# Kernel optimization log

Measured on AMD Instinct MI355X. Metric: run time of the kernel, lower is better.

The kernel has to match this reference:

```python
import jax, jax.numpy as jnp
import numpy as np

H_IMG, W_IMG = 60, 80          # hardcoded grid in get_positional_encodings
NUM_HEADS = 8
DIM = 256
N_TOK = H_IMG * W_IMG          # 4800

# Hardcoded intrinsics in the source: fx=517/9, fy=517/8, cx=40, cy=30.
# fx_norm = fx/(2*cx)*2, fy_norm = fy/(2*cy)*2 ; cx_norm = cy_norm = 0,
# so Kinv is diagonal and Kinv @ [x, y, 1] = [x/fx_n, y/fy_n, 1].
_FX_N = (517.0 / 9.0) / 80.0 * 2.0
_FY_N = (517.0 / 8.0) / 60.0 * 2.0


def _positional(B):
    ys = jnp.linspace(-1.0, 1.0, H_IMG)
    xs = jnp.linspace(-1.0, 1.0, W_IMG)
    # loop index j*w + k: y varies over rows (outer), x over cols (inner)
    p3 = jnp.repeat(ys, W_IMG) / _FY_N   # (N,) = y'/w'
    p4 = jnp.tile(xs, H_IMG) / _FX_N     # (N,) = x'/w'
    pos = jnp.stack([p3 * p3, p4 * p4, p3 * p4, p3, p4, jnp.ones_like(p3)], axis=-1)  # (N,6)
    return jnp.broadcast_to(pos, (B, N_TOK, 6))


def setup_inputs() -> dict:
    key = jax.random.key(0)
    k1, k2, k3, k4, k5 = jax.random.split(key, 5)
    B, N, C, H = 1, N_TOK, DIM, NUM_HEADS
    return {
        "x1": jax.random.normal(k1, (B, N, C), dtype=jnp.float32),
        "x2": jax.random.normal(k2, (B, N, C), dtype=jnp.float32),
        "qkv_w": jax.random.normal(k3, (3 * C, C), dtype=jnp.float32) * 0.02,
        "proj_w": jax.random.normal(k4, (C, C + 6 * H), dtype=jnp.float32) * 0.02,
        "proj_b": jax.random.normal(k5, (C,), dtype=jnp.float32) * 0.02,
    }


def reference(x1, x2, qkv_w, proj_w, proj_b):
    B, N, C = x1.shape
    H = NUM_HEADS
    hd = C // H
    scale = hd ** -0.5
    D = hd + 6

    def qkv(x):
        y = (x @ qkv_w.T).reshape(B, N, 3, H, hd).transpose(2, 0, 3, 1, 4)
        return y[0], y[1], y[2]   # each (B,H,N,hd)

    q1, k1, v1 = qkv(x1)
    q2, k2, v2 = qkv(x2)

    pos_h = jnp.broadcast_to(_positional(B)[:, None], (B, H, N, 6))

    def fundamental(q, k, v):
        a = jnp.einsum('bhnd,bhmd->bhnm', q, k) * scale          # (B,H,N,N)
        af = jax.nn.softmax(a, axis=-1) * jax.nn.softmax(a, axis=-2)  # dual softmax
        vc = jnp.concatenate([v, pos_h], axis=-1)                 # (B,H,N,D)
        f = jnp.einsum('bhnc,bhnm->bhcm', vc, af)                 # V^T A
        f = jnp.einsum('bhcm,bhmd->bhcd', f, vc)                  # (V^T A) V -> (B,H,D,D)
        f = f.reshape(B, H * D, D).transpose(0, 2, 1)             # (B, D, H*D)
        return f @ proj_w.T + proj_b                              # (B, D, C)

    fundamental_1 = fundamental(q2, k1, v1)
    fundamental_2 = fundamental(q1, k2, v2)
    return fundamental_2, fundamental_1
```

## Files before the change

### kernel.cpp

```cpp
#include <hip/hip_runtime.h>
#include <stdint.h>
#include <math.h>

#define N_TOK 4800
#define NH 8
#define HD 32
#define DP 40
#define DD 38
#define NTILES 150
#define MCHUNK 3
#define FRAG 2048
#define SCALE 0.17677669529663687f
#define QSCALE (0.17677669529663687f * 1.4426950408889634f)

typedef float f32x16 __attribute__((ext_vector_type(16)));
typedef short s8v __attribute__((ext_vector_type(8)));
typedef int i2v __attribute__((ext_vector_type(2)));

#if __has_builtin(__builtin_amdgcn_exp2f)
#define EXP2F(x) __builtin_amdgcn_exp2f(x)
#else
#define EXP2F(x) exp2f(x)
#endif

__device__ __forceinline__ unsigned short f2bf(float x) {
    union { float f; uint32_t u; } v; v.f = x;
    uint32_t r = v.u + 0x7FFFu + ((v.u >> 16) & 1u);
    return (unsigned short)(r >> 16);
}
__device__ __forceinline__ int cvtpk(float lo, float hi) {
    int r;
    asm("v_cvt_pk_bf16_f32 %0, %1, %2" : "=v"(r) : "v"(lo), "v"(hi));
    return r;
}
__device__ __forceinline__ s8v mk_s8(int a, int b, int c, int d) {
    union { int i[4]; s8v s; } u;
    u.i[0] = a; u.i[1] = b; u.i[2] = c; u.i[3] = d;
    return u.s;
}
__device__ __forceinline__ float posv(int m, int idx) {
    const int rrow = m / 80, rcol = m % 80;
    const float y = -1.0f + (float)rrow * (2.0f / 59.0f);
    const float x = -1.0f + (float)rcol * (2.0f / 79.0f);
    const float p3 = y * (240.0f / 517.0f);
    const float p4 = x * (360.0f / 517.0f);
    if (idx == 0) return p3 * p3;
    if (idx == 1) return p4 * p4;
    if (idx == 2) return p3 * p4;
    if (idx == 3) return p3;
    if (idx == 4) return p4;
    return 1.0f;
}

template<int NX, int NY, int NZ>
__device__ __forceinline__ void swzdec(int& x, int& y, int& z) {
    const int L = blockIdx.x + NX * (blockIdx.y + NY * blockIdx.z);
    constexpr int cpx = NX * NY * NZ / 8;
    const int s = (L & 7) * cpx + (L >> 3);
    x = s % NX;
    const int r = s / NX;
    y = r % NY;
    z = r / NY;
}
template<int NX, int NY, int NZ>
__device__ __forceinline__ void swzdec_xo(int& x, int& y, int& z) {
    const int L = blockIdx.x + NX * (blockIdx.y + NY * blockIdx.z);
    constexpr int cpx = NX * NY * NZ / 8;
    const int s = (L & 7) * cpx + (L >> 3);
    x = s / (NY * NZ);
    const int r = s % (NY * NZ);
    y = r % NY;
    z = r / NY;
}

#define MFMA(a, b, c) __builtin_amdgcn_mfma_f32_32x32x16_bf16((a), (b), (c), 0, 0, 0)

__global__ __launch_bounds__(256) void frag_kernel(
    const float* __restrict__ x1, unsigned short* __restrict__ xh1,
    const float* __restrict__ x2, unsigned short* __restrict__ xh2,
    const float* __restrict__ w, unsigned short* __restrict__ wh)
{
    int b = blockIdx.x;
    const float* src; unsigned short* dh;
    if (b < 150)      { src = x1 + b * 8192; dh = xh1 + b * 8192; }
    else if (b < 300) { b -= 150; src = x2 + b * 8192; dh = xh2 + b * 8192; }
    else              { b -= 300; src = w + b * 8192; dh = wh + b * 8192; }
    const int t = threadIdx.x;
#pragma unroll
    for (int k = 0; k < 4; ++k) {
        const int f = k * 256 + t;
        const int c = f >> 6;
        const int rem = f & 63;
        const float* sp = src + (rem & 31) * 256 + c * 16 + (rem >> 5) * 8;
        const float4 a = *(const float4*)(sp);
        const float4 bb = *(const float4*)(sp + 4);
        const float vv[8] = {a.x, a.y, a.z, a.w, bb.x, bb.y, bb.z, bb.w};
        union { unsigned short s[8]; s8v v; } H;
#pragma unroll
        for (int j = 0; j < 8; ++j) H.s[j] = f2bf(vv[j]);
        *(s8v*)(dh + f * 8) = H.v;
    }
}

__global__ __launch_bounds__(128, 4) void qkv_mfma_kernel(
    const unsigned short* __restrict__ xhA, unsigned short* __restrict__ qbA,
    unsigned short* __restrict__ kbA, float* __restrict__ vcbA,
    const unsigned short* __restrict__ xhB, unsigned short* __restrict__ qbB,
    unsigned short* __restrict__ kbB, float* __restrict__ vcbB,
    const unsigned short* __restrict__ wh)
{
    __shared__ float tlbuf[2][32][33];
    int bx, by, bz;
    swzdec_xo<75, 12, 2>(bx, by, bz);
    const int sel = bz;
    const unsigned short* xh = sel ? xhB : xhA;
    unsigned short* qb = sel ? qbB : qbA;
    unsigned short* kb = sel ? kbB : kbA;
    float* vcb = sel ? vcbB : vcbA;
    const int lane = threadIdx.x & 63;
    const int wid = threadIdx.x >> 6;
    const int xtile = bx * 2 + wid;
    const unsigned short* xp = xh + (size_t)xtile * 8192 + lane * 8;
    const unsigned short* wp0 = wh + (size_t)(by * 2) * 8192 + lane * 8;
    const unsigned short* wp1 = wp0 + 8192;
    f32x16 acc0 = {}, acc1 = {};
#pragma unroll
    for (int c = 0; c < 16; ++c) {
        const s8v aH = *(const s8v*)(xp + c * 512);
        const s8v b0 = *(const s8v*)(wp0 + c * 512);
        const s8v b1 = *(const s8v*)(wp1 + c * 512);
        acc0 = MFMA(aH, b0, acc0);
        acc1 = MFMA(aH, b1, acc1);
    }
    const int lr = lane & 31, hi5 = lane >> 5;
    const int row = lane >> 1, ch = (lane & 1) * 16;
    float (*T)[33] = tlbuf[wid];
#pragma unroll
    for (int jj = 0; jj < 2; ++jj) {
#pragma unroll
        for (int r = 0; r < 16; ++r) {
            const float v = jj ? acc1[r] : acc0[r];
            T[(r & 3) + 8 * (r >> 2) + 4 * hi5][lr] = v;
        }
        const int jt = by * 2 + jj, s = jt >> 3, h = jt & 7;
        const int n = xtile * 32 + row;
        if (s == 2) {
            float4* dst = (float4*)&vcb[(size_t)(h * N_TOK + n) * HD + ch];
#pragma unroll
            for (int k = 0; k < 4; ++k) {
                dst[k] = make_float4(T[row][ch + 4 * k + 0], T[row][ch + 4 * k + 1],
                                     T[row][ch + 4 * k + 2], T[row][ch + 4 * k + 3]);
            }
        } else {
            const float m = (s == 0) ? QSCALE : 1.0f;
            unsigned short* dst = (s == 0 ? qb : kb)
                                  + (size_t)(h * N_TOK + n) * HD + ch;
            union { unsigned short u[8]; s8v v; } o0, o1;
#pragma unroll
            for (int i = 0; i < 8; ++i) {
                o0.u[i] = f2bf(T[row][ch + i] * m);
                o1.u[i] = f2bf(T[row][ch + 8 + i] * m);
            }
            *(s8v*)dst = o0.v;
            *(s8v*)(dst + 8) = o1.v;
        }
    }
}

__global__ __launch_bounds__(192, 4) void cs_kernel(
    const unsigned short* __restrict__ qbA, const unsigned short* __restrict__ kbA,
    float* __restrict__ csA,
    const unsigned short* __restrict__ qbB, const unsigned short* __restrict__ kbB,
    float* __restrict__ csB)
{
    int bx, by, bz;
    swzdec<50, 5, 16>(bx, by, bz);
    const int sel = bz >> 3;
    const unsigned short* qb = sel ? qbB : qbA;
    const unsigned short* kb = sel ? kbB : kbA;
    float* cs = sel ? csB : csA;
    const int lane = threadIdx.x & 63;
    const int wid = threadIdx.x >> 6;
    const int h = bz & 7;
    const int m0 = bx * 96 + wid * 32;
    const int lr = lane & 31, hi5 = lane >> 5;
    const int hbase = h * N_TOK;
    const unsigned short* kp = kb + (hbase + m0 + lr) * HD + 8 * hi5;
    const s8v bK0 = *(const s8v*)(kp);
    const s8v bK1 = *(const s8v*)(kp + 16);
    const unsigned short* qp = qb + (hbase + by * 960 + lr) * HD + 8 * hi5;
    s8v a0 = *(const s8v*)(qp);
    s8v a1 = *(const s8v*)(qp + 16);
    float csa = 0.f, csb = 0.f;
#pragma unroll 2
    for (int it = 0; it < 30; ++it) {
        qp += 32 * HD;
        const s8v na0 = *(const s8v*)(qp);
        const s8v na1 = *(const s8v*)(qp + 16);
        f32x16 acc = {};
        acc = MFMA(a0, bK0, acc);
        acc = MFMA(a1, bK1, acc);
#pragma unroll
        for (int r = 0; r < 16; r += 2) {
            csa += EXP2F(acc[r]);
            csb += EXP2F(acc[r + 1]);
        }
        a0 = na0; a1 = na1;
    }
    float csacc = csa + csb;
    csacc += __shfl_xor(csacc, 32);
    if (lane < 32) atomicAdd(&cs[hbase + m0 + lane], csacc);
}

__global__ __launch_bounds__(256) void vfrag_kernel(
    const float* __restrict__ vcA, const float* __restrict__ csA,
    unsigned short* __restrict__ vfA,
    const float* __restrict__ vcB, const float* __restrict__ csB,
    unsigned short* __restrict__ vfB)
{
    const int sel = blockIdx.y >> 3;
    const float* vc = sel ? vcB : vcA;
    const float* cs = sel ? csB : csA;
    unsigned short* vf = sel ? vfB : vfA;
    __shared__ float vl[32][33];
    __shared__ float ul[32];
    const int mt = blockIdx.x;
    const int h = blockIdx.y & 7;
    const int t = threadIdx.x;
    const int m0 = mt * 32;
    const float* vcbase = vc + (size_t)(h * N_TOK + m0) * HD;
    for (int e = t; e < 32 * HD; e += 256) vl[e >> 5][e & 31] = vcbase[e];
    if (t < 32) ul[t] = 1.0f / cs[(size_t)h * N_TOK + m0 + t];
    __syncthreads();
    const int b = t >> 6, lane = t & 63;
    const int hi5 = lane >> 5, lr = lane & 31;
    const int d = (b >> 1) * 32 + lr;
    const int mb = (b & 1) * 16 + hi5 * 8;
    union { unsigned short s[8]; s8v v; } pk;
#pragma unroll
    for (int j = 0; j < 8; ++j) {
        const int mo = mb + j;
        float v;
        if (d < 32)      v = vl[mo][d];
        else if (d < 38) v = posv(m0 + mo, d - 32);
        else             v = 0.0f;
        pk.s[j] = f2bf(v * ul[mo]);
    }
    *(s8v*)(vf + ((size_t)(h * NTILES + mt) * 4 + b) * 512 + lane * 8) = pk.v;
}

__global__ __launch_bounds__(192, 4) void tprime_mfma_kernel(
    const unsigned short* __restrict__ qbA, const unsigned short* __restrict__ kbA,
    const unsigned short* __restrict__ vfA, float* __restrict__ rsA,
    float* __restrict__ TA0, float* __restrict__ TA1, float* __restrict__ TA2,
    const unsigned short* __restrict__ qbB, const unsigned short* __restrict__ kbB,
    const unsigned short* __restrict__ vfB, float* __restrict__ rsB,
    float* __restrict__ TB0, float* __restrict__ TB1, float* __restrict__ TB2)
{
    int bx, by, bz;
    swzdec<50, MCHUNK, 16>(bx, by, bz);
    const int sel = bz >> 3;
    const unsigned short* qb = sel ? qbB : qbA;
    const unsigned short* kb = sel ? kbB : kbA;
    const unsigned short* vf = sel ? vfB : vfA;
    float* rs = sel ? rsB : rsA;
    float* T = sel ? (by == 0 ? TB0 : (by == 1 ? TB1 : TB2))
                   : (by == 0 ? TA0 : (by == 1 ? TA1 : TA2));
    const int lane = threadIdx.x & 63;
    const int wid = threadIdx.x >> 6;
    const int h = bz & 7;
    const int n0 = bx * 96 + wid * 32;
    const int lr = lane & 31, hi5 = lane >> 5;
    const int hbase = h * N_TOK;
    const unsigned short* qp = qb + (hbase + n0 + lr) * HD + 8 * hi5;
    const s8v bQ0 = *(const s8v*)(qp);
    const s8v bQ1 = *(const s8v*)(qp + 16);
    f32x16 t0 = {}, t1 = {};
    float rsa = 0.f, rsb = 0.f;
    const int mt0 = by * 50;
    const unsigned short* kp = kb + (hbase + mt0 * 32 + lr) * HD + 8 * hi5;
    const unsigned short* vp = vf + (size_t)(h * NTILES + mt0) * FRAG + lane * 8;
    s8v a0 = *(const s8v*)(kp);
    s8v a1 = *(const s8v*)(kp + 16);
    s8v v00 = *(const s8v*)(vp);
    s8v v01 = *(const s8v*)(vp + 512);
    s8v v10 = *(const s8v*)(vp + 1024);
    s8v v11 = *(const s8v*)(vp + 1536);
#pragma unroll 2
    for (int it = 0; it < 50; ++it) {
        kp += 32 * HD; vp += FRAG;
        const s8v na0 = *(const s8v*)(kp);
        const s8v na1 = *(const s8v*)(kp + 16);
        const s8v nv00 = *(const s8v*)(vp);
        const s8v nv01 = *(const s8v*)(vp + 512);
        const s8v nv10 = *(const s8v*)(vp + 1024);
        const s8v nv11 = *(const s8v*)(vp + 1536);
        f32x16 s = {};
        s = MFMA(a0, bQ0, s);
        s = MFMA(a1, bQ1, s);
        float p[16];
#pragma unroll
        for (int r = 0; r < 16; r += 2) {
            const float e0 = EXP2F(s[r]);
            const float e1 = EXP2F(s[r + 1]);
            rsa += e0; rsb += e1;
            p[r] = e0 * e0; p[r + 1] = e1 * e1;
        }
        const int L0 = cvtpk(p[0], p[1]),   L1 = cvtpk(p[2], p[3]);
        const int H0 = cvtpk(p[4], p[5]),   H1 = cvtpk(p[6], p[7]);
        const int L2 = cvtpk(p[8], p[9]),   L3 = cvtpk(p[10], p[11]);
        const int H2 = cvtpk(p[12], p[13]), H3 = cvtpk(p[14], p[15]);
        const i2v s0 = __builtin_amdgcn_permlane32_swap(L0, H0, false, false);
        const i2v s1 = __builtin_amdgcn_permlane32_swap(L1, H1, false, false);
        const i2v s2 = __builtin_amdgcn_permlane32_swap(L2, H2, false, false);
        const i2v s3 = __builtin_amdgcn_permlane32_swap(L3, H3, false, false);
        const s8v pa0 = mk_s8(s0[0], s1[0], s0[1], s1[1]);
        const s8v pa1 = mk_s8(s2[0], s3[0], s2[1], s3[1]);
        __builtin_amdgcn_s_setprio(1);
        t0 = MFMA(pa0, v00, t0);
        t0 = MFMA(pa1, v01, t0);
        t1 = MFMA(pa0, v10, t1);
        t1 = MFMA(pa1, v11, t1);
        __builtin_amdgcn_s_setprio(0);
        a0 = na0; a1 = na1;
        v00 = nv00; v01 = nv01; v10 = nv10; v11 = nv11;
    }
    float rsacc = rsa + rsb;
    rsacc += __shfl_xor(rsacc, 32);
    if (lane < 32) atomicAdd(&rs[hbase + n0 + lane], rsacc);
#pragma unroll
    for (int r = 0; r < 16; ++r) {
        const int n = n0 + (r & 3) + 8 * (r >> 2) + 4 * hi5;
        T[(size_t)(hbase + n) * DP + lr] = t0[r];
    }
    if (lr < 8) {
#pragma unroll
        for (int r = 0; r < 16; ++r) {
            const int n = n0 + (r & 3) + 8 * (r >> 2) + 4 * hi5;
            T[(size_t)(hbase + n) * DP + 32 + lr] = t1[r];
        }
    }
}

__global__ __launch_bounds__(256) void fgemm_kernel(
    const float* __restrict__ VCA, const float* __restrict__ rsA,
    const float* __restrict__ TA0, const float* __restrict__ TA1,
    const float* __restrict__ TA2, float* __restrict__ fA,
    const float* __restrict__ VCB, const float* __restrict__ rsB,
    const float* __restrict__ TB0, const float* __restrict__ TB1,
    const float* __restrict__ TB2, float* __restrict__ fB)
{
    const int sel = blockIdx.x >> 3;
    const float* VC = sel ? VCB : VCA;
    const float* rs = sel ? rsB : rsA;
    const float* Ta = sel ? TB0 : TA0;
    const float* Tb = sel ? TB1 : TA1;
    const float* Tc = sel ? TB2 : TA2;
    float* f = sel ? fB : fA;
    __shared__ __align__(16) float wvcl[64 * DP];
    __shared__ __align__(16) float tl[64 * DP];
    __shared__ float wl[64];
    const int h = blockIdx.x & 7, n0 = blockIdx.y * 64;
    const int t = threadIdx.x;
    if (t < 64) wl[t] = 1.0f / rs[(size_t)h * N_TOK + n0 + t];
    __syncthreads();
    const float* vcbase = VC + (size_t)(h * N_TOK + n0) * HD;
    const float* tabase = Ta + (size_t)(h * N_TOK + n0) * DP;
    const float* tbbase = Tb + (size_t)(h * N_TOK + n0) * DP;
    const float* tcbase = Tc + (size_t)(h * N_TOK + n0) * DP;
    for (int e = t; e < 64 * DP; e += 256) {
        const int row = e / DP, c = e - row * DP;
        float v;
        if (c < 32)      v = vcbase[row * HD + c];
        else if (c < 38) v = posv(n0 + row, c - 32);
        else             v = 0.0f;
        wvcl[e] = v * wl[row];
        tl[e] = tabase[e] + tbbase[e] + tcbase[e];
    }
    __syncthreads();
    for (int p = t; p < DD * DD; p += 256) {
        const int c = p / DD, d = p % DD;
        float s = 0.f;
#pragma unroll 8
        for (int n = 0; n < 64; ++n) s += wvcl[n * DP + c] * tl[n * DP + d];
        atomicAdd(&f[(size_t)(h * DD + c) * DP + d], s);
    }
}

__global__ __launch_bounds__(256) void out_kernel(
    const float* __restrict__ f1, const float* __restrict__ f2,
    const float* __restrict__ pw, const float* __restrict__ pb,
    float* __restrict__ out)
{
    const int sel = blockIdx.y;
    const float* f = sel ? f2 : f1;
    float* dst = sel ? out : (out + DD * 256);
    __shared__ __align__(16) float flds[304];
    const int d = blockIdx.x, t = threadIdx.x;
    for (int j = t; j < 304; j += 256) flds[j] = f[(size_t)j * DP + d];
    __syncthreads();
    float acc = pb[t];
    const float* pwrow = pw + (size_t)t * 304;
#pragma unroll 4
    for (int j = 0; j < 304; j += 4) {
        const float4 p4 = *(const float4*)&pwrow[j];
        const float4 f4 = *(const float4*)&flds[j];
        acc += p4.x * f4.x + p4.y * f4.y + p4.z * f4.z + p4.w * f4.w;
    }
    dst[(size_t)d * 256 + t] = acc;
}

extern "C" void kernel_launch(void* const* d_in, const int* in_sizes, int n_in,
                              void* d_out, int out_size, void* d_ws, size_t ws_size,
                              hipStream_t stream)
{
    const float* x1 = (const float*)d_in[0];
    const float* x2 = (const float*)d_in[1];
    const float* qkv_w = (const float*)d_in[2];
    const float* proj_w = (const float*)d_in[3];
    const float* proj_b = (const float*)d_in[4];
    float* out = (float*)d_out;

    const size_t QSZ = (size_t)NH * N_TOK * HD;
    const size_t VSZ = (size_t)NH * N_TOK * DP;
    const size_t SSZ = (size_t)NH * N_TOK;
    const size_t FSZ = (size_t)NH * DD * DP;
    const size_t XSZ = (size_t)N_TOK * 256;
    const size_t WSZ = (size_t)768 * 256;
    const size_t VTSZ = (size_t)NH * NTILES * FRAG;

    float* vc1 = (float*)d_ws;
    float* vc2 = vc1 + QSZ;
    float* rs1 = vc2 + QSZ;
    float* cs1 = rs1 + SSZ;
    float* rs2 = cs1 + SSZ;
    float* cs2 = rs2 + SSZ;
    float* f1 = cs2 + SSZ;
    float* f2 = f1 + FSZ;
    float* T1a = f2 + FSZ;
    float* T1b = T1a + VSZ;
    float* T1c = T1b + VSZ;
    float* T2a = T1c + VSZ;
    float* T2b = T2a + VSZ;
    float* T2c = T2b + VSZ;
    unsigned short* xh1 = (unsigned short*)(T2c + VSZ);
    unsigned short* xh2 = xh1 + XSZ;
    unsigned short* wh = xh2 + XSZ;
    unsigned short* qb1 = wh + WSZ;
    unsigned short* kb1 = qb1 + QSZ;
    unsigned short* qb2 = kb1 + QSZ;
    unsigned short* kb2 = qb2 + QSZ;
    unsigned short* vf1 = kb2 + QSZ;
    unsigned short* vf2 = vf1 + VTSZ;

    const size_t zbytes = (4 * SSZ + 2 * FSZ) * sizeof(float);
    hipMemsetAsync(rs1, 0, zbytes, stream);

    frag_kernel<<<324, 256, 0, stream>>>(x1, xh1, x2, xh2, qkv_w, wh);

    qkv_mfma_kernel<<<dim3(75, 12, 2), 128, 0, stream>>>(
        xh1, qb1, kb1, vc1, xh2, qb2, kb2, vc2, wh);

    cs_kernel<<<dim3(50, 5, 16), 192, 0, stream>>>(qb2, kb1, cs1,
                                                   qb1, kb2, cs2);
    vfrag_kernel<<<dim3(150, 16), 256, 0, stream>>>(vc1, cs1, vf1,
                                                    vc2, cs2, vf2);
    tprime_mfma_kernel<<<dim3(50, MCHUNK, 16), 192, 0, stream>>>(
        qb2, kb1, vf1, rs1, T1a, T1b, T1c,
        qb1, kb2, vf2, rs2, T2a, T2b, T2c);
    fgemm_kernel<<<dim3(16, 75), 256, 0, stream>>>(
        vc1, rs1, T1a, T1b, T1c, f1,
        vc2, rs2, T2a, T2b, T2c, f2);
    out_kernel<<<dim3(38, 2), 256, 0, stream>>>(f1, f2, proj_w, proj_b, out);
}
```

Measured before the change: 221.4 us.

## Store T partials in bf16, fold memset into frag kernel, widen cs tiles

The T partial buffers written by tprime and read by fgemm are now stored as packed bf16 instead of fp32, which halves that intermediate traffic at some cost in accumulation precision. The hipMemsetAsync is replaced by extra blocks in frag_kernel that zero the accumulator buffers, removing one launch. cs_kernel now handles 64 key columns per wave with two MFMA accumulators, halving the grid and reusing each Q fragment load twice.

```diff
diff --git a/kernel.cpp b/kernel.cpp
--- a/kernel.cpp
+++ b/kernel.cpp
@@ -27,6 +27,10 @@
     union { float f; uint32_t u; } v; v.f = x;
     uint32_t r = v.u + 0x7FFFu + ((v.u >> 16) & 1u);
     return (unsigned short)(r >> 16);
+}
+__device__ __forceinline__ float bf2f(unsigned short h) {
+    union { uint32_t u; float f; } v; v.u = ((uint32_t)h) << 16;
+    return v.f;
 }
 __device__ __forceinline__ int cvtpk(float lo, float hi) {
     int r;
@@ -78,14 +82,20 @@
 __global__ __launch_bounds__(256) void frag_kernel(
     const float* __restrict__ x1, unsigned short* __restrict__ xh1,
     const float* __restrict__ x2, unsigned short* __restrict__ xh2,
-    const float* __restrict__ w, unsigned short* __restrict__ wh)
+    const float* __restrict__ w, unsigned short* __restrict__ wh,
+    float* __restrict__ zbase, int zn4)
 {
     int b = blockIdx.x;
+    const int t = threadIdx.x;
+    if (b >= 324) {
+        const int i = (b - 324) * 256 + t;
+        if (i < zn4) ((float4*)zbase)[i] = make_float4(0.f, 0.f, 0.f, 0.f);
+        return;
+    }
     const float* src; unsigned short* dh;
     if (b < 150)      { src = x1 + b * 8192; dh = xh1 + b * 8192; }
     else if (b < 300) { b -= 150; src = x2 + b * 8192; dh = xh2 + b * 8192; }
     else              { b -= 300; src = w + b * 8192; dh = wh + b * 8192; }
-    const int t = threadIdx.x;
 #pragma unroll
     for (int k = 0; k < 4; ++k) {
         const int f = k * 256 + t;
@@ -174,7 +184,7 @@
     float* __restrict__ csB)
 {
     int bx, by, bz;
-    swzdec<50, 5, 16>(bx, by, bz);
+    swzdec<25, 5, 16>(bx, by, bz);
     const int sel = bz >> 3;
     const unsigned short* qb = sel ? qbB : qbA;
     const unsigned short* kb = sel ? kbB : kbA;
@@ -182,34 +192,44 @@
     const int lane = threadIdx.x & 63;
     const int wid = threadIdx.x >> 6;
     const int h = bz & 7;
-    const int m0 = bx * 96 + wid * 32;
+    const int m0 = bx * 192 + wid * 64;
     const int lr = lane & 31, hi5 = lane >> 5;
     const int hbase = h * N_TOK;
     const unsigned short* kp = kb + (hbase + m0 + lr) * HD + 8 * hi5;
     const s8v bK0 = *(const s8v*)(kp);
     const s8v bK1 = *(const s8v*)(kp + 16);
+    const s8v bK2 = *(const s8v*)(kp + 32 * HD);
+    const s8v bK3 = *(const s8v*)(kp + 32 * HD + 16);
     const unsigned short* qp = qb + (hbase + by * 960 + lr) * HD + 8 * hi5;
     s8v a0 = *(const s8v*)(qp);
     s8v a1 = *(const s8v*)(qp + 16);
-    float csa = 0.f, csb = 0.f;
+    float c0 = 0.f, c1 = 0.f, c2 = 0.f, c3 = 0.f;
 #pragma unroll 2
     for (int it = 0; it < 30; ++it) {
         qp += 32 * HD;
         const s8v na0 = *(const s8v*)(qp);
         const s8v na1 = *(const s8v*)(qp + 16);
-        f32x16 acc = {};
-        acc = MFMA(a0, bK0, acc);
-        acc = MFMA(a1, bK1, acc);
+        f32x16 accA = {}, accB = {};
+        accA = MFMA(a0, bK0, accA);
+        accB = MFMA(a0, bK2, accB);
+        accA = MFMA(a1, bK1, accA);
+        accB = MFMA(a1, bK3, accB);
 #pragma unroll
         for (int r = 0; r < 16; r += 2) {
-            csa += EXP2F(acc[r]);
-            csb += EXP2F(acc[r + 1]);
+            c0 += EXP2F(accA[r]);
+            c1 += EXP2F(accA[r + 1]);
+            c2 += EXP2F(accB[r]);
+            c3 += EXP2F(accB[r + 1]);
         }
         a0 = na0; a1 = na1;
     }
-    float csacc = csa + csb;
-    csacc += __shfl_xor(csacc, 32);
-    if (lane < 32) atomicAdd(&cs[hbase + m0 + lane], csacc);
+    float cA = c0 + c1, cB = c2 + c3;
+    cA += __shfl_xor(cA, 32);
+    cB += __shfl_xor(cB, 32);
+    if (lane < 32) {
+        atomicAdd(&cs[hbase + m0 + lane], cA);
+        atomicAdd(&cs[hbase + m0 + 32 + lane], cB);
+    }
 }
 
 __global__ __launch_bounds__(256) void vfrag_kernel(
@@ -252,10 +272,12 @@
 __global__ __launch_bounds__(192, 4) void tprime_mfma_kernel(
     const unsigned short* __restrict__ qbA, const unsigned short* __restrict__ kbA,
     const unsigned short* __restrict__ vfA, float* __restrict__ rsA,
-    float* __restrict__ TA0, float* __restrict__ TA1, float* __restrict__ TA2,
+    unsigned short* __restrict__ TA0, unsigned short* __restrict__ TA1,
+    unsigned short* __restrict__ TA2,
     const unsigned short* __restrict__ qbB, const unsigned short* __restrict__ kbB,
     const unsigned short* __restrict__ vfB, float* __restrict__ rsB,
-    float* __restrict__ TB0, float* __restrict__ TB1, float* __restrict__ TB2)
+    unsigned short* __restrict__ TB0, unsigned short* __restrict__ TB1,
+    unsigned short* __restrict__ TB2)
 {
     int bx, by, bz;
     swzdec<50, MCHUNK, 16>(bx, by, bz);
@@ -264,8 +286,8 @@
     const unsigned short* kb = sel ? kbB : kbA;
     const unsigned short* vf = sel ? vfB : vfA;
     float* rs = sel ? rsB : rsA;
-    float* T = sel ? (by == 0 ? TB0 : (by == 1 ? TB1 : TB2))
-                   : (by == 0 ? TA0 : (by == 1 ? TA1 : TA2));
+    unsigned short* T = sel ? (by == 0 ? TB0 : (by == 1 ? TB1 : TB2))
+                            : (by == 0 ? TA0 : (by == 1 ? TA1 : TA2));
     const int lane = threadIdx.x & 63;
     const int wid = threadIdx.x >> 6;
     const int h = bz & 7;
@@ -328,34 +350,36 @@
     float rsacc = rsa + rsb;
     rsacc += __shfl_xor(rsacc, 32);
     if (lane < 32) atomicAdd(&rs[hbase + n0 + lane], rsacc);
+    unsigned int* Tw = (unsigned int*)T;
 #pragma unroll
     for (int r = 0; r < 16; ++r) {
         const int n = n0 + (r & 3) + 8 * (r >> 2) + 4 * hi5;
-        T[(size_t)(hbase + n) * DP + lr] = t0[r];
-    }
-    if (lr < 8) {
-#pragma unroll
-        for (int r = 0; r < 16; ++r) {
-            const int n = n0 + (r & 3) + 8 * (r >> 2) + 4 * hi5;
-            T[(size_t)(hbase + n) * DP + 32 + lr] = t1[r];
+        const float par0 = __shfl_xor(t0[r], 1);
+        const float par1 = __shfl_xor(t1[r], 1);
+        if (!(lr & 1)) {
+            Tw[(size_t)(hbase + n) * (DP / 2) + (lr >> 1)] =
+                (unsigned int)cvtpk(t0[r], par0);
+            if (lr < 8)
+                Tw[(size_t)(hbase + n) * (DP / 2) + 16 + (lr >> 1)] =
+                    (unsigned int)cvtpk(t1[r], par1);
         }
     }
 }
 
 __global__ __launch_bounds__(256) void fgemm_kernel(
     const float* __restrict__ VCA, const float* __restrict__ rsA,
-    const float* __restrict__ TA0, const float* __restrict__ TA1,
-    const float* __restrict__ TA2, float* __restrict__ fA,
+    const unsigned short* __restrict__ TA0, const unsigned short* __restrict__ TA1,
+    const unsigned short* __restrict__ TA2, float* __restrict__ fA,
     const float* __restrict__ VCB, const float* __restrict__ rsB,
-    const float* __restrict__ TB0, const float* __restrict__ TB1,
-    const float* __restrict__ TB2, float* __restrict__ fB)
+    const unsigned short* __restrict__ TB0, const unsigned short* __restrict__ TB1,
+    const unsigned short* __restrict__ TB2, float* __restrict__ fB)
 {
     const int sel = blockIdx.x >> 3;
     const float* VC = sel ? VCB : VCA;
     const float* rs = sel ? rsB : rsA;
-    const float* Ta = sel ? TB0 : TA0;
-    const float* Tb = sel ? TB1 : TA1;
-    const float* Tc = sel ? TB2 : TA2;
+    const unsigned short* Ta = sel ? TB0 : TA0;
+    const unsigned short* Tb = sel ? TB1 : TA1;
+    const unsigned short* Tc = sel ? TB2 : TA2;
     float* f = sel ? fB : fA;
     __shared__ __align__(16) float wvcl[64 * DP];
     __shared__ __align__(16) float tl[64 * DP];
@@ -365,9 +389,18 @@
     if (t < 64) wl[t] = 1.0f / rs[(size_t)h * N_TOK + n0 + t];
     __syncthreads();
     const float* vcbase = VC + (size_t)(h * N_TOK + n0) * HD;
-    const float* tabase = Ta + (size_t)(h * N_TOK + n0) * DP;
-    const float* tbbase = Tb + (size_t)(h * N_TOK + n0) * DP;
-    const float* tcbase = Tc + (size_t)(h * N_TOK + n0) * DP;
+    const ushort4* ta4 = (const ushort4*)(Ta + (size_t)(h * N_TOK + n0) * DP);
+    const ushort4* tb4 = (const ushort4*)(Tb + (size_t)(h * N_TOK + n0) * DP);
+    const ushort4* tc4 = (const ushort4*)(Tc + (size_t)(h * N_TOK + n0) * DP);
+    for (int e4 = t; e4 < 64 * DP / 4; e4 += 256) {
+        const ushort4 a4 = ta4[e4];
+        const ushort4 b4 = tb4[e4];
+        const ushort4 c4 = tc4[e4];
+        tl[e4 * 4 + 0] = bf2f(a4.x) + bf2f(b4.x) + bf2f(c4.x);
+        tl[e4 * 4 + 1] = bf2f(a4.y) + bf2f(b4.y) + bf2f(c4.y);
+        tl[e4 * 4 + 2] = bf2f(a4.z) + bf2f(b4.z) + bf2f(c4.z);
+        tl[e4 * 4 + 3] = bf2f(a4.w) + bf2f(b4.w) + bf2f(c4.w);
+    }
     for (int e = t; e < 64 * DP; e += 256) {
         const int row = e / DP, c = e - row * DP;
         float v;
@@ -375,7 +408,6 @@
         else if (c < 38) v = posv(n0 + row, c - 32);
         else             v = 0.0f;
         wvcl[e] = v * wl[row];
-        tl[e] = tabase[e] + tbbase[e] + tcbase[e];
     }
     __syncthreads();
     for (int p = t; p < DD * DD; p += 256) {
@@ -437,13 +469,7 @@
     float* cs2 = rs2 + SSZ;
     float* f1 = cs2 + SSZ;
     float* f2 = f1 + FSZ;
-    float* T1a = f2 + FSZ;
-    float* T1b = T1a + VSZ;
-    float* T1c = T1b + VSZ;
-    float* T2a = T1c + VSZ;
-    float* T2b = T2a + VSZ;
-    float* T2c = T2b + VSZ;
-    unsigned short* xh1 = (unsigned short*)(T2c + VSZ);
+    unsigned short* xh1 = (unsigned short*)(f2 + FSZ);
     unsigned short* xh2 = xh1 + XSZ;
     unsigned short* wh = xh2 + XSZ;
     unsigned short* qb1 = wh + WSZ;
@@ -452,16 +478,22 @@
     unsigned short* kb2 = qb2 + QSZ;
     unsigned short* vf1 = kb2 + QSZ;
     unsigned short* vf2 = vf1 + VTSZ;
-
-    const size_t zbytes = (4 * SSZ + 2 * FSZ) * sizeof(float);
-    hipMemsetAsync(rs1, 0, zbytes, stream);
-
-    frag_kernel<<<324, 256, 0, stream>>>(x1, xh1, x2, xh2, qkv_w, wh);
+    unsigned short* T1a = vf2 + VTSZ;
+    unsigned short* T1b = T1a + VSZ;
+    unsigned short* T1c = T1b + VSZ;
+    unsigned short* T2a = T1c + VSZ;
+    unsigned short* T2b = T2a + VSZ;
+    unsigned short* T2c = T2b + VSZ;
+
+    const int zn4 = (int)((4 * SSZ + 2 * FSZ) / 4);
+
+    frag_kernel<<<324 + 174, 256, 0, stream>>>(x1, xh1, x2, xh2, qkv_w, wh,
+                                               rs1, zn4);
 
     qkv_mfma_kernel<<<dim3(75, 12, 2), 128, 0, stream>>>(
         xh1, qb1, kb1, vc1, xh2, qb2, kb2, vc2, wh);
 
-    cs_kernel<<<dim3(50, 5, 16), 192, 0, stream>>>(qb2, kb1, cs1,
+    cs_kernel<<<dim3(25, 5, 16), 192, 0, stream>>>(qb2, kb1, cs1,
                                                    qb1, kb2, cs2);
     vfrag_kernel<<<dim3(150, 16), 256, 0, stream>>>(vc1, cs1, vf1,
                                                     vc2, cs2, vf2);
```

New measurement: 212.5 us. 1.04x faster.
